# Performance work log

Hardware: AMD Instinct MI355X
Metric: run time of the kernel (lower is better)

Reference implementation:

```python
import jax, jax.numpy as jnp
import numpy as np
import math

B, S, D, H = 2, 2048, 1024, 16

def setup_inputs() -> dict:
    key = jax.random.key(0)
    ks = jax.random.split(key, 13)
    def lin(kw, kb, out_d, in_d):
        W = jax.random.normal(kw, (out_d, in_d), dtype=jnp.float32) * 0.02
        b = jax.random.normal(kb, (out_d,), dtype=jnp.float32) * 0.02
        return W, b
    Wq, bq = lin(ks[0], ks[1], D, D)
    Wk, bk = lin(ks[2], ks[3], D, D)
    Wv, bv = lin(ks[4], ks[5], D, D)
    Wo, bo = lin(ks[6], ks[7], D, D)
    query = jax.random.normal(ks[8], (B, S, D), dtype=jnp.float32)
    key_t = jax.random.normal(ks[9], (B, S, D), dtype=jnp.float32)
    value = jax.random.normal(ks[10], (B, S, D), dtype=jnp.float32)
    src_mask = jax.random.randint(ks[11], (B, S), 0, 2).astype(bool)  # True = masked out
    return {"query": query, "key": key_t, "value": value, "src_mask": src_mask,
            "Wq": Wq, "bq": bq, "Wk": Wk, "bk": bk, "Wv": Wv, "bv": bv,
            "Wo": Wo, "bo": bo, "nhead": H}

def reference(query, key, value, src_mask, Wq, bq, Wk, bk, Wv, bv, Wo, bo, nhead):
    b, s, d = query.shape
    hd = d // nhead
    scale = 1.0 / math.sqrt(hd)
    def split_heads(x):  # [b,s,d] -> [b,h,s,hd]
        return x.reshape(b, -1, nhead, hd).transpose(0, 2, 1, 3)
    q = split_heads(query @ Wq.T + bq)
    k = split_heads(key @ Wk.T + bk)
    v = split_heads(value @ Wv.T + bv)
    scores = jnp.einsum('bhqe,bhke->bhqk', q, k) * scale  # [b,h,s,s]
    # mask True -> -9e9, broadcast over heads and query positions (matches repeat)
    scores = jnp.where(src_mask[:, None, None, :], jnp.float32(-9e9), scores)
    probs = jax.nn.softmax(scores, axis=-1)
    # dropout is identity in eval mode
    out = jnp.einsum('bhqk,bhke->bhqe', probs, v)  # [b,h,s,hd]
    out = out.transpose(0, 2, 1, 3).reshape(b, s, d)
    out = out @ Wo.T + bo
    return out
```

## Files before the change

### kernel.cpp

```cpp
#include <hip/hip_runtime.h>
#include <hip/hip_bf16.h>
#include <cstdint>
#include <cstddef>

#define B_ 2
#define S_ 2048
#define D_ 1024
#define H_ 16
#define HD_ 64
#define M_ 4096

typedef __attribute__((ext_vector_type(8))) short short8;
typedef __attribute__((ext_vector_type(4))) short shortx4;
typedef __attribute__((ext_vector_type(4))) float floatx4;

__device__ __forceinline__ floatx4 mfma32(short8 a, short8 b, floatx4 c) {
    return __builtin_amdgcn_mfma_f32_16x16x32_bf16(a, b, c, 0, 0, 0);
}
__device__ __forceinline__ floatx4 mfma16(shortx4 a, shortx4 b, floatx4 c) {
    return __builtin_amdgcn_mfma_f32_16x16x16bf16_1k(a, b, c, 0, 0, 0);
}

__device__ __forceinline__ void gload_lds16(const __hip_bfloat16* g, __hip_bfloat16* lds_base) {
    __builtin_amdgcn_global_load_lds(
        (const __attribute__((address_space(1))) void*)g,
        (__attribute__((address_space(3))) void*)lds_base, 16, 0, 0);
}

__global__ __launch_bounds__(256) void cvt3_kernel(
    const float* __restrict__ a, const float* __restrict__ b, const float* __restrict__ c,
    __hip_bfloat16* __restrict__ dst, int n)
{
    const float* src = blockIdx.z == 0 ? a : blockIdx.z == 1 ? b : c;
    __hip_bfloat16* d = dst + (size_t)blockIdx.z * n;
    int i = (blockIdx.x * 256 + threadIdx.x) * 4;
    float4 v = *(const float4*)(src + i);
    union { __hip_bfloat16 h[4]; uint2 u; } cv;
    cv.h[0] = __float2bfloat16(v.x); cv.h[1] = __float2bfloat16(v.y);
    cv.h[2] = __float2bfloat16(v.z); cv.h[3] = __float2bfloat16(v.w);
    *(uint2*)(d + i) = cv.u;
}

__global__ __launch_bounds__(256) void cvt4_kernel(
    const float* __restrict__ a, const float* __restrict__ b,
    const float* __restrict__ c, const float* __restrict__ e,
    __hip_bfloat16* __restrict__ dst, int n)
{
    const float* src = blockIdx.z == 0 ? a : blockIdx.z == 1 ? b : blockIdx.z == 2 ? c : e;
    __hip_bfloat16* d = dst + (size_t)blockIdx.z * n;
    int i = (blockIdx.x * 256 + threadIdx.x) * 4;
    float4 v = *(const float4*)(src + i);
    union { __hip_bfloat16 h[4]; uint2 u; } cv;
    cv.h[0] = __float2bfloat16(v.x); cv.h[1] = __float2bfloat16(v.y);
    cv.h[2] = __float2bfloat16(v.z); cv.h[3] = __float2bfloat16(v.w);
    *(uint2*)(d + i) = cv.u;
}

template <int MODE>
__device__ __forceinline__ void gemm_core(
    const __hip_bfloat16* __restrict__ A,
    const __hip_bfloat16* __restrict__ W,
    const float* __restrict__ bias,
    void* __restrict__ Cout,
    __hip_bfloat16* __restrict__ smem,
    int m0, int n0, int N)
{
    __hip_bfloat16* As = smem;
    __hip_bfloat16* Bs = smem + 128 * 32;
    const int K = D_;
    const int tid  = threadIdx.x;
    const int wave = tid >> 6;
    const int lane = tid & 63;
    const int quad = lane >> 4;
    const int l15  = lane & 15;
    const int wm   = (wave & 1) * 64;
    const int wn   = (wave >> 1) * 64;
    const int srow = lane >> 2;
    const int scol = (lane & 3) * 8;

    floatx4 acc[4][4];
#pragma unroll
    for (int i = 0; i < 4; i++)
#pragma unroll
        for (int j = 0; j < 4; j++) {
            floatx4 z = {0.f, 0.f, 0.f, 0.f};
            acc[i][j] = z;
        }

    for (int k0 = 0; k0 < K; k0 += 32) {
        __syncthreads();
#pragma unroll
        for (int t = 0; t < 2; t++) {
            int r0 = wave * 32 + t * 16;
            gload_lds16(A + (size_t)(m0 + r0 + srow) * K + k0 + scol, As + r0 * 32);
            gload_lds16(W + (size_t)(n0 + r0 + srow) * K + k0 + scol, Bs + r0 * 32);
        }
        __syncthreads();

        short8 afr[4], bfr[4];
#pragma unroll
        for (int i = 0; i < 4; i++)
            afr[i] = *(const short8*)(As + (wm + i * 16 + l15) * 32 + quad * 8);
#pragma unroll
        for (int j = 0; j < 4; j++)
            bfr[j] = *(const short8*)(Bs + (wn + j * 16 + l15) * 32 + quad * 8);
#pragma unroll
        for (int i = 0; i < 4; i++)
#pragma unroll
            for (int j = 0; j < 4; j++)
                acc[i][j] = mfma32(afr[i], bfr[j], acc[i][j]);
    }

    if constexpr (MODE == 1) {
#pragma unroll
        for (int j = 0; j < 4; j++) {
            int col = n0 + wn + j * 16 + l15;
            int h = col >> 6, e = col & 63;
            float bv = bias[col];
#pragma unroll
            for (int i = 0; i < 4; i++) {
                int s0 = m0 + wm + i * 16 + quad * 4;
                int bb = s0 >> 11, sl = s0 & 2047;
                union { __hip_bfloat16 hx[4]; uint2 u; } pk;
#pragma unroll
                for (int r = 0; r < 4; r++)
                    pk.hx[r] = __float2bfloat16(acc[i][j][r] + bv);
                *(uint2*)((__hip_bfloat16*)Cout + (((size_t)bb * H_ + h) * HD_ + e) * S_ + sl) = pk.u;
            }
        }
    } else {
#pragma unroll
        for (int j = 0; j < 4; j++) {
            int col = n0 + wn + j * 16 + l15;
            float bv = bias[col];
#pragma unroll
            for (int i = 0; i < 4; i++) {
#pragma unroll
                for (int r = 0; r < 4; r++) {
                    int rowg = m0 + wm + i * 16 + quad * 4 + r;
                    ((__hip_bfloat16*)Cout)[(size_t)rowg * N + col] =
                        __float2bfloat16(acc[i][j][r] + bv);
                }
            }
        }
    }
}

__global__ __launch_bounds__(256) void qkv_gemm_kernel(
    const __hip_bfloat16* __restrict__ qb, const __hip_bfloat16* __restrict__ kb,
    const __hip_bfloat16* __restrict__ vb,
    const __hip_bfloat16* __restrict__ Wqb, const __hip_bfloat16* __restrict__ Wkb,
    const __hip_bfloat16* __restrict__ Wvb,
    const float* __restrict__ bq, const float* __restrict__ bk, const float* __restrict__ bv,
    __hip_bfloat16* __restrict__ Qp, __hip_bfloat16* __restrict__ Kp,
    __hip_bfloat16* __restrict__ Vt)
{
    __shared__ __hip_bfloat16 smem[2 * 128 * 32] __attribute__((aligned(16)));
    const int z = blockIdx.z;
    const __hip_bfloat16* A = z == 0 ? qb : z == 1 ? kb : vb;
    const __hip_bfloat16* W = z == 0 ? Wqb : z == 1 ? Wkb : Wvb;
    const float* bias = z == 0 ? bq : z == 1 ? bk : bv;
    int m0 = blockIdx.y * 128, n0 = blockIdx.x * 128;
    if (z < 2) gemm_core<0>(A, W, bias, z == 0 ? (void*)Qp : (void*)Kp, smem, m0, n0, D_);
    else       gemm_core<1>(A, W, bias, (void*)Vt, smem, m0, n0, D_);
}

__global__ __launch_bounds__(256) void oproj_gemm_kernel(
    const __hip_bfloat16* __restrict__ A, const __hip_bfloat16* __restrict__ W,
    const float* __restrict__ bias, float* __restrict__ out)
{
    __shared__ __hip_bfloat16 As[64 * 32]  __attribute__((aligned(16)));
    __shared__ __hip_bfloat16 Bs[128 * 32] __attribute__((aligned(16)));
    const int K = D_, N = D_;
    const int tid  = threadIdx.x;
    const int m0   = blockIdx.y * 64;
    const int n0   = blockIdx.x * 128;
    const int wave = tid >> 6;
    const int lane = tid & 63;
    const int quad = lane >> 4;
    const int l15  = lane & 15;
    const int wm   = (wave & 1) * 32;
    const int wn   = (wave >> 1) * 64;
    const int srow = lane >> 2;
    const int scol = (lane & 3) * 8;

    floatx4 acc[2][4];
#pragma unroll
    for (int i = 0; i < 2; i++)
#pragma unroll
        for (int j = 0; j < 4; j++) {
            floatx4 z = {0.f, 0.f, 0.f, 0.f};
            acc[i][j] = z;
        }

    for (int k0 = 0; k0 < K; k0 += 32) {
        __syncthreads();
        {
            int ra = wave * 16;
            gload_lds16(A + (size_t)(m0 + ra + srow) * K + k0 + scol, As + ra * 32);
#pragma unroll
            for (int t = 0; t < 2; t++) {
                int rb = wave * 32 + t * 16;
                gload_lds16(W + (size_t)(n0 + rb + srow) * K + k0 + scol, Bs + rb * 32);
            }
        }
        __syncthreads();

        short8 afr[2], bfr[4];
#pragma unroll
        for (int i = 0; i < 2; i++)
            afr[i] = *(const short8*)(As + (wm + i * 16 + l15) * 32 + quad * 8);
#pragma unroll
        for (int j = 0; j < 4; j++)
            bfr[j] = *(const short8*)(Bs + (wn + j * 16 + l15) * 32 + quad * 8);
#pragma unroll
        for (int i = 0; i < 2; i++)
#pragma unroll
            for (int j = 0; j < 4; j++)
                acc[i][j] = mfma32(afr[i], bfr[j], acc[i][j]);
    }

#pragma unroll
    for (int j = 0; j < 4; j++) {
        int col = n0 + wn + j * 16 + l15;
        float bv = bias[col];
#pragma unroll
        for (int i = 0; i < 2; i++) {
#pragma unroll
            for (int r = 0; r < 4; r++) {
                int rowg = m0 + wm + i * 16 + quad * 4 + r;
                out[(size_t)rowg * N + col] = acc[i][j][r] + bv;
            }
        }
    }
}

#define LDP 72
__global__ __launch_bounds__(512) void flash_attn_kernel(
    const __hip_bfloat16* __restrict__ Q,
    const __hip_bfloat16* __restrict__ Kp,
    const __hip_bfloat16* __restrict__ Vt,
    const int* __restrict__ mask,
    __hip_bfloat16* __restrict__ O)
{
    __shared__ __hip_bfloat16 Qs [128 * LDP] __attribute__((aligned(16)));
    __shared__ __hip_bfloat16 Ks [64 * LDP]  __attribute__((aligned(16)));
    __shared__ __hip_bfloat16 Vts[64 * LDP]  __attribute__((aligned(16)));

    const int tid  = threadIdx.x;
    const int q0   = blockIdx.x * 128;
    const int bh   = blockIdx.y;
    const int b    = bh >> 4;
    const int h    = bh & 15;
    const int wave = tid >> 6;
    const int lane = tid & 63;
    const int quad = lane >> 4;
    const int l15  = lane & 15;
    const float kSc = 0.18033688f;

    const size_t baseQ = ((size_t)b * S_ + q0) * D_ + (size_t)h * HD_;
#pragma unroll
    for (int c = tid; c < 1024; c += 512) {
        int row = c >> 3, kc = c & 7;
        *(uint4*)(Qs + row * LDP + kc * 8) = *(const uint4*)(Q + baseQ + (size_t)row * D_ + kc * 8);
    }
    __syncthreads();

    short8 qb[2];
    qb[0] = *(const short8*)(Qs + (wave * 16 + l15) * LDP + quad * 8);
    qb[1] = *(const short8*)(Qs + (wave * 16 + l15) * LDP + 32 + quad * 8);

    float lsum = 0.f;
    floatx4 o_acc[4];
#pragma unroll
    for (int ot = 0; ot < 4; ot++) {
        floatx4 z = {0.f, 0.f, 0.f, 0.f};
        o_acc[ot] = z;
    }

    const int* mrow = mask + b * S_;
    const __hip_bfloat16* VtBase = Vt + (size_t)bh * HD_ * S_;

    for (int kv0 = 0; kv0 < S_; kv0 += 64) {
        __syncthreads();
        const size_t baseK = ((size_t)b * S_ + kv0) * D_ + (size_t)h * HD_;
        {
            int row = tid >> 3, kc = tid & 7;
            *(uint4*)(Ks + row * LDP + kc * 8) =
                *(const uint4*)(Kp + baseK + (size_t)row * D_ + kc * 8);
            *(uint4*)(Vts + row * LDP + kc * 8) =
                *(const uint4*)(VtBase + (size_t)row * S_ + kv0 + kc * 8);
        }
        __syncthreads();

        int4 mq[4];
#pragma unroll
        for (int nt = 0; nt < 4; nt++)
            mq[nt] = *(const int4*)(mrow + kv0 + nt * 16 + quad * 4);

        floatx4 s_acc[4];
#pragma unroll
        for (int nt = 0; nt < 4; nt++) {
            short8 kb0 = *(const short8*)(Ks + (nt * 16 + l15) * LDP + quad * 8);
            short8 kb1 = *(const short8*)(Ks + (nt * 16 + l15) * LDP + 32 + quad * 8);
            floatx4 z = {0.f, 0.f, 0.f, 0.f};
            z = mfma32(kb0, qb[0], z);
            z = mfma32(kb1, qb[1], z);
            s_acc[nt] = z;
        }

        shortx4 pf[4];
#pragma unroll
        for (int nt = 0; nt < 4; nt++) {
            float pe0 = mq[nt].x ? 0.f : __builtin_amdgcn_exp2f(s_acc[nt][0] * kSc);
            float pe1 = mq[nt].y ? 0.f : __builtin_amdgcn_exp2f(s_acc[nt][1] * kSc);
            float pe2 = mq[nt].z ? 0.f : __builtin_amdgcn_exp2f(s_acc[nt][2] * kSc);
            float pe3 = mq[nt].w ? 0.f : __builtin_amdgcn_exp2f(s_acc[nt][3] * kSc);
            lsum += (pe0 + pe1) + (pe2 + pe3);
            union { shortx4 s4; __hip_bfloat162 b2[2]; } pk;
            pk.b2[0] = __float22bfloat162_rn({pe0, pe1});
            pk.b2[1] = __float22bfloat162_rn({pe2, pe3});
            pf[nt] = pk.s4;
        }

#pragma unroll
        for (int nt = 0; nt < 4; nt++) {
#pragma unroll
            for (int ot = 0; ot < 4; ot++) {
                shortx4 vb = *(const shortx4*)(Vts + (ot * 16 + l15) * LDP + nt * 16 + quad * 4);
                o_acc[ot] = mfma16(pf[nt], vb, o_acc[ot]);
            }
        }
    }

    lsum += __shfl_xor(lsum, 16);
    lsum += __shfl_xor(lsum, 32);

    const size_t baseO = ((size_t)b * S_ + q0) * D_ + (size_t)h * HD_;
#pragma unroll
    for (int r = 0; r < 4; r++) {
        float inv = 1.0f / __shfl(lsum, quad * 4 + r);
        int rowl = wave * 16 + quad * 4 + r;
#pragma unroll
        for (int ot = 0; ot < 4; ot++)
            O[baseO + (size_t)rowl * D_ + ot * 16 + l15] =
                __float2bfloat16(o_acc[ot][r] * inv);
    }
}

extern "C" void kernel_launch(void* const* d_in, const int* in_sizes, int n_in,
                              void* d_out, int out_size, void* d_ws, size_t ws_size,
                              hipStream_t stream) {
    const float* query = (const float*)d_in[0];
    const float* key   = (const float*)d_in[1];
    const float* value = (const float*)d_in[2];
    const int*   mask  = (const int*)d_in[3];
    const float* Wq    = (const float*)d_in[4];
    const float* bq    = (const float*)d_in[5];
    const float* Wk    = (const float*)d_in[6];
    const float* bk    = (const float*)d_in[7];
    const float* Wv    = (const float*)d_in[8];
    const float* bv    = (const float*)d_in[9];
    const float* Wo    = (const float*)d_in[10];
    const float* bo    = (const float*)d_in[11];
    float* out = (float*)d_out;

    const size_t SZ_IN = (size_t)M_ * D_;
    const size_t SZ_W  = (size_t)D_ * D_;
    __hip_bfloat16* qb  = (__hip_bfloat16*)d_ws;
    __hip_bfloat16* kb  = qb  + SZ_IN;
    __hip_bfloat16* vb  = kb  + SZ_IN;
    __hip_bfloat16* Wqb = vb  + SZ_IN;
    __hip_bfloat16* Wkb = Wqb + SZ_W;
    __hip_bfloat16* Wvb = Wkb + SZ_W;
    __hip_bfloat16* Wob = Wvb + SZ_W;
    __hip_bfloat16* Qp  = Wob + SZ_W;
    __hip_bfloat16* Kp  = Qp  + SZ_IN;
    __hip_bfloat16* Vt  = Kp  + SZ_IN;

    cvt3_kernel<<<dim3(SZ_IN / 1024, 1, 3), 256, 0, stream>>>(query, key, value, qb, (int)SZ_IN);
    cvt4_kernel<<<dim3(SZ_W / 1024, 1, 4), 256, 0, stream>>>(Wq, Wk, Wv, Wo, Wqb, (int)SZ_W);

    qkv_gemm_kernel<<<dim3(D_ / 128, M_ / 128, 3), 256, 0, stream>>>(
        qb, kb, vb, Wqb, Wkb, Wvb, bq, bk, bv, Qp, Kp, Vt);

    flash_attn_kernel<<<dim3(S_ / 128, B_ * H_), 512, 0, stream>>>(Qp, Kp, Vt, mask, Qp);

    oproj_gemm_kernel<<<dim3(D_ / 128, M_ / 64), 256, 0, stream>>>(Qp, Wob, bo, out);
}
```

Baseline: 242.4 us.

## Double-buffer K/V tiles in flash attention with register prefetch and 2 row-groups per wave

Rewrites the attention loop to prefetch the next K/V tile and mask into registers while computing the current one, storing into a second LDS buffer so each iteration needs one barrier instead of two. Block size drops from 512 to 256 threads, so each wave now handles two 16-row query groups and reuses each K/V LDS fragment across both. It also raises wave priority around the MFMA sections. The cost is more registers per thread and double the K/V LDS footprint, which may reduce occupancy.

```diff
diff --git a/kernel.cpp b/kernel.cpp
--- a/kernel.cpp
+++ b/kernel.cpp
@@ -236,16 +236,17 @@
 }
 
 #define LDP 72
-__global__ __launch_bounds__(512) void flash_attn_kernel(
+#define NT_ (S_ / 64)
+__global__ __launch_bounds__(256) void flash_attn_kernel(
     const __hip_bfloat16* __restrict__ Q,
     const __hip_bfloat16* __restrict__ Kp,
     const __hip_bfloat16* __restrict__ Vt,
     const int* __restrict__ mask,
     __hip_bfloat16* __restrict__ O)
 {
-    __shared__ __hip_bfloat16 Qs [128 * LDP] __attribute__((aligned(16)));
-    __shared__ __hip_bfloat16 Ks [64 * LDP]  __attribute__((aligned(16)));
-    __shared__ __hip_bfloat16 Vts[64 * LDP]  __attribute__((aligned(16)));
+    __shared__ __hip_bfloat16 Qs  [128 * LDP]    __attribute__((aligned(16)));
+    __shared__ __hip_bfloat16 KsB [2][64 * LDP]  __attribute__((aligned(16)));
+    __shared__ __hip_bfloat16 VtsB[2][64 * LDP]  __attribute__((aligned(16)));
 
     const int tid  = threadIdx.x;
     const int q0   = blockIdx.x * 128;
@@ -260,91 +261,132 @@
 
     const size_t baseQ = ((size_t)b * S_ + q0) * D_ + (size_t)h * HD_;
 #pragma unroll
-    for (int c = tid; c < 1024; c += 512) {
+    for (int c = tid; c < 1024; c += 256) {
         int row = c >> 3, kc = c & 7;
         *(uint4*)(Qs + row * LDP + kc * 8) = *(const uint4*)(Q + baseQ + (size_t)row * D_ + kc * 8);
     }
-    __syncthreads();
-
-    short8 qb[2];
-    qb[0] = *(const short8*)(Qs + (wave * 16 + l15) * LDP + quad * 8);
-    qb[1] = *(const short8*)(Qs + (wave * 16 + l15) * LDP + 32 + quad * 8);
-
-    float lsum = 0.f;
-    floatx4 o_acc[4];
-#pragma unroll
-    for (int ot = 0; ot < 4; ot++) {
-        floatx4 z = {0.f, 0.f, 0.f, 0.f};
-        o_acc[ot] = z;
-    }
 
     const int* mrow = mask + b * S_;
     const __hip_bfloat16* VtBase = Vt + (size_t)bh * HD_ * S_;
-
-    for (int kv0 = 0; kv0 < S_; kv0 += 64) {
-        __syncthreads();
-        const size_t baseK = ((size_t)b * S_ + kv0) * D_ + (size_t)h * HD_;
-        {
-            int row = tid >> 3, kc = tid & 7;
-            *(uint4*)(Ks + row * LDP + kc * 8) =
-                *(const uint4*)(Kp + baseK + (size_t)row * D_ + kc * 8);
-            *(uint4*)(Vts + row * LDP + kc * 8) =
-                *(const uint4*)(VtBase + (size_t)row * S_ + kv0 + kc * 8);
-        }
-        __syncthreads();
+    const size_t baseKrow = (size_t)b * S_ * D_ + (size_t)h * HD_;
+
+    const int r0  = tid >> 3;
+    const int r1  = r0 + 32;
+    const int kc0 = (tid & 7) * 8;
+
+    uint4 kreg0, kreg1, vreg0, vreg1;
+    int4  mreg[4];
+
+    auto issue = [&](int kv0) {
+        kreg0 = *(const uint4*)(Kp + baseKrow + (size_t)(kv0 + r0) * D_ + kc0);
+        kreg1 = *(const uint4*)(Kp + baseKrow + (size_t)(kv0 + r1) * D_ + kc0);
+        vreg0 = *(const uint4*)(VtBase + (size_t)r0 * S_ + kv0 + kc0);
+        vreg1 = *(const uint4*)(VtBase + (size_t)r1 * S_ + kv0 + kc0);
+#pragma unroll
+        for (int nt = 0; nt < 4; nt++)
+            mreg[nt] = *(const int4*)(mrow + kv0 + nt * 16 + quad * 4);
+    };
+    auto commit = [&](int pb) {
+        *(uint4*)(KsB[pb]  + r0 * LDP + kc0) = kreg0;
+        *(uint4*)(KsB[pb]  + r1 * LDP + kc0) = kreg1;
+        *(uint4*)(VtsB[pb] + r0 * LDP + kc0) = vreg0;
+        *(uint4*)(VtsB[pb] + r1 * LDP + kc0) = vreg1;
+    };
+
+    issue(0);
+    commit(0);
+    __syncthreads();
+
+    short8 qb[2][2];
+#pragma unroll
+    for (int g = 0; g < 2; g++) {
+        qb[g][0] = *(const short8*)(Qs + (wave * 32 + g * 16 + l15) * LDP + quad * 8);
+        qb[g][1] = *(const short8*)(Qs + (wave * 32 + g * 16 + l15) * LDP + 32 + quad * 8);
+    }
+
+    float lsum[2] = {0.f, 0.f};
+    floatx4 o_acc[2][4];
+#pragma unroll
+    for (int g = 0; g < 2; g++)
+#pragma unroll
+        for (int ot = 0; ot < 4; ot++) {
+            floatx4 z = {0.f, 0.f, 0.f, 0.f};
+            o_acc[g][ot] = z;
+        }
+
+    for (int t = 0; t < NT_; ++t) {
+        if (t) __syncthreads();
 
         int4 mq[4];
 #pragma unroll
-        for (int nt = 0; nt < 4; nt++)
-            mq[nt] = *(const int4*)(mrow + kv0 + nt * 16 + quad * 4);
-
-        floatx4 s_acc[4];
+        for (int nt = 0; nt < 4; nt++) mq[nt] = mreg[nt];
+
+        if (t + 1 < NT_) issue((t + 1) * 64);
+
+        const __hip_bfloat16* Ks  = KsB [t & 1];
+        const __hip_bfloat16* Vts = VtsB[t & 1];
+
+        floatx4 s_acc[2][4];
+        __builtin_amdgcn_s_setprio(1);
 #pragma unroll
         for (int nt = 0; nt < 4; nt++) {
             short8 kb0 = *(const short8*)(Ks + (nt * 16 + l15) * LDP + quad * 8);
             short8 kb1 = *(const short8*)(Ks + (nt * 16 + l15) * LDP + 32 + quad * 8);
-            floatx4 z = {0.f, 0.f, 0.f, 0.f};
-            z = mfma32(kb0, qb[0], z);
-            z = mfma32(kb1, qb[1], z);
-            s_acc[nt] = z;
-        }
-
-        shortx4 pf[4];
-#pragma unroll
-        for (int nt = 0; nt < 4; nt++) {
-            float pe0 = mq[nt].x ? 0.f : __builtin_amdgcn_exp2f(s_acc[nt][0] * kSc);
-            float pe1 = mq[nt].y ? 0.f : __builtin_amdgcn_exp2f(s_acc[nt][1] * kSc);
-            float pe2 = mq[nt].z ? 0.f : __builtin_amdgcn_exp2f(s_acc[nt][2] * kSc);
-            float pe3 = mq[nt].w ? 0.f : __builtin_amdgcn_exp2f(s_acc[nt][3] * kSc);
-            lsum += (pe0 + pe1) + (pe2 + pe3);
-            union { shortx4 s4; __hip_bfloat162 b2[2]; } pk;
-            pk.b2[0] = __float22bfloat162_rn({pe0, pe1});
-            pk.b2[1] = __float22bfloat162_rn({pe2, pe3});
-            pf[nt] = pk.s4;
-        }
-
-#pragma unroll
-        for (int nt = 0; nt < 4; nt++) {
+#pragma unroll
+            for (int g = 0; g < 2; g++) {
+                floatx4 z = {0.f, 0.f, 0.f, 0.f};
+                z = mfma32(kb0, qb[g][0], z);
+                z = mfma32(kb1, qb[g][1], z);
+                s_acc[g][nt] = z;
+            }
+        }
+        __builtin_amdgcn_s_setprio(0);
+
+        shortx4 pf[2][4];
+#pragma unroll
+        for (int g = 0; g < 2; g++)
+#pragma unroll
+            for (int nt = 0; nt < 4; nt++) {
+                float pe0 = mq[nt].x ? 0.f : __builtin_amdgcn_exp2f(s_acc[g][nt][0] * kSc);
+                float pe1 = mq[nt].y ? 0.f : __builtin_amdgcn_exp2f(s_acc[g][nt][1] * kSc);
+                float pe2 = mq[nt].z ? 0.f : __builtin_amdgcn_exp2f(s_acc[g][nt][2] * kSc);
+                float pe3 = mq[nt].w ? 0.f : __builtin_amdgcn_exp2f(s_acc[g][nt][3] * kSc);
+                lsum[g] += (pe0 + pe1) + (pe2 + pe3);
+                union { shortx4 s4; __hip_bfloat162 b2[2]; } pk;
+                pk.b2[0] = __float22bfloat162_rn({pe0, pe1});
+                pk.b2[1] = __float22bfloat162_rn({pe2, pe3});
+                pf[g][nt] = pk.s4;
+            }
+
+        __builtin_amdgcn_s_setprio(1);
+#pragma unroll
+        for (int nt = 0; nt < 4; nt++)
 #pragma unroll
             for (int ot = 0; ot < 4; ot++) {
                 shortx4 vb = *(const shortx4*)(Vts + (ot * 16 + l15) * LDP + nt * 16 + quad * 4);
-                o_acc[ot] = mfma16(pf[nt], vb, o_acc[ot]);
-            }
-        }
-    }
-
-    lsum += __shfl_xor(lsum, 16);
-    lsum += __shfl_xor(lsum, 32);
-
-    const size_t baseO = ((size_t)b * S_ + q0) * D_ + (size_t)h * HD_;
-#pragma unroll
-    for (int r = 0; r < 4; r++) {
-        float inv = 1.0f / __shfl(lsum, quad * 4 + r);
-        int rowl = wave * 16 + quad * 4 + r;
-#pragma unroll
-        for (int ot = 0; ot < 4; ot++)
-            O[baseO + (size_t)rowl * D_ + ot * 16 + l15] =
-                __float2bfloat16(o_acc[ot][r] * inv);
+                o_acc[0][ot] = mfma16(pf[0][nt], vb, o_acc[0][ot]);
+                o_acc[1][ot] = mfma16(pf[1][nt], vb, o_acc[1][ot]);
+            }
+        __builtin_amdgcn_s_setprio(0);
+
+        if (t + 1 < NT_) commit((t + 1) & 1);
+    }
+
+    const size_t baseO = baseQ;
+#pragma unroll
+    for (int g = 0; g < 2; g++) {
+        float ls = lsum[g];
+        ls += __shfl_xor(ls, 16);
+        ls += __shfl_xor(ls, 32);
+#pragma unroll
+        for (int r = 0; r < 4; r++) {
+            float inv = 1.0f / __shfl(ls, quad * 4 + r);
+            int rowl = wave * 32 + g * 16 + quad * 4 + r;
+#pragma unroll
+            for (int ot = 0; ot < 4; ot++)
+                O[baseO + (size_t)rowl * D_ + ot * 16 + l15] =
+                    __float2bfloat16(o_acc[g][ot][r] * inv);
+        }
     }
 }
 
@@ -384,7 +426,7 @@
     qkv_gemm_kernel<<<dim3(D_ / 128, M_ / 128, 3), 256, 0, stream>>>(
         qb, kb, vb, Wqb, Wkb, Wvb, bq, bk, bv, Qp, Kp, Vt);
 
-    flash_attn_kernel<<<dim3(S_ / 128, B_ * H_), 512, 0, stream>>>(Qp, Kp, Vt, mask, Qp);
+    flash_attn_kernel<<<dim3(S_ / 128, B_ * H_), 256, 0, stream>>>(Qp, Kp, Vt, mask, Qp);
 
     oproj_gemm_kernel<<<dim3(D_ / 128, M_ / 64), 256, 0, stream>>>(Qp, Wob, bo, out);
 }
```

Measured after the change: 239.1 us. Within noise of the previous version (-1.4%).

## Double-buffer K/V tiles in flash attention with register prefetch

Applied to the files above, without the earlier changes.

The attention loop now uses two LDS buffers for K and V^T tiles. Global loads for the next tile, including the mask, go into registers before the current tile's MFMAs and are written to the other buffer afterwards, which drops one barrier per iteration. MFMA sections are also wrapped in s_setprio to raise wave priority. The aim is to hide global-load latency behind compute, at the cost of extra LDS and registers.

```diff
diff --git a/kernel.cpp b/kernel.cpp
--- a/kernel.cpp
+++ b/kernel.cpp
@@ -236,6 +236,7 @@
 }
 
 #define LDP 72
+#define NT_ (S_ / 64)
 __global__ __launch_bounds__(512) void flash_attn_kernel(
     const __hip_bfloat16* __restrict__ Q,
     const __hip_bfloat16* __restrict__ Kp,
@@ -243,9 +244,9 @@
     const int* __restrict__ mask,
     __hip_bfloat16* __restrict__ O)
 {
-    __shared__ __hip_bfloat16 Qs [128 * LDP] __attribute__((aligned(16)));
-    __shared__ __hip_bfloat16 Ks [64 * LDP]  __attribute__((aligned(16)));
-    __shared__ __hip_bfloat16 Vts[64 * LDP]  __attribute__((aligned(16)));
+    __shared__ __hip_bfloat16 Qs  [128 * LDP]    __attribute__((aligned(16)));
+    __shared__ __hip_bfloat16 KsB [2][64 * LDP]  __attribute__((aligned(16)));
+    __shared__ __hip_bfloat16 VtsB[2][64 * LDP]  __attribute__((aligned(16)));
 
     const int tid  = threadIdx.x;
     const int q0   = blockIdx.x * 128;
@@ -264,6 +265,31 @@
         int row = c >> 3, kc = c & 7;
         *(uint4*)(Qs + row * LDP + kc * 8) = *(const uint4*)(Q + baseQ + (size_t)row * D_ + kc * 8);
     }
+
+    const int* mrow = mask + b * S_;
+    const __hip_bfloat16* VtBase = Vt + (size_t)bh * HD_ * S_;
+    const size_t baseKrow = (size_t)b * S_ * D_ + (size_t)h * HD_;
+
+    const int r0  = tid >> 3;
+    const int kc0 = (tid & 7) * 8;
+
+    uint4 kreg, vreg;
+    int4  mreg[4];
+
+    auto issue = [&](int kv0) {
+        kreg = *(const uint4*)(Kp + baseKrow + (size_t)(kv0 + r0) * D_ + kc0);
+        vreg = *(const uint4*)(VtBase + (size_t)r0 * S_ + kv0 + kc0);
+#pragma unroll
+        for (int nt = 0; nt < 4; nt++)
+            mreg[nt] = *(const int4*)(mrow + kv0 + nt * 16 + quad * 4);
+    };
+    auto commit = [&](int pb) {
+        *(uint4*)(KsB[pb]  + r0 * LDP + kc0) = kreg;
+        *(uint4*)(VtsB[pb] + r0 * LDP + kc0) = vreg;
+    };
+
+    issue(0);
+    commit(0);
     __syncthreads();
 
     short8 qb[2];
@@ -278,27 +304,20 @@
         o_acc[ot] = z;
     }
 
-    const int* mrow = mask + b * S_;
-    const __hip_bfloat16* VtBase = Vt + (size_t)bh * HD_ * S_;
-
-    for (int kv0 = 0; kv0 < S_; kv0 += 64) {
-        __syncthreads();
-        const size_t baseK = ((size_t)b * S_ + kv0) * D_ + (size_t)h * HD_;
-        {
-            int row = tid >> 3, kc = tid & 7;
-            *(uint4*)(Ks + row * LDP + kc * 8) =
-                *(const uint4*)(Kp + baseK + (size_t)row * D_ + kc * 8);
-            *(uint4*)(Vts + row * LDP + kc * 8) =
-                *(const uint4*)(VtBase + (size_t)row * S_ + kv0 + kc * 8);
-        }
-        __syncthreads();
+    for (int t = 0; t < NT_; ++t) {
+        if (t) __syncthreads();
 
         int4 mq[4];
 #pragma unroll
-        for (int nt = 0; nt < 4; nt++)
-            mq[nt] = *(const int4*)(mrow + kv0 + nt * 16 + quad * 4);
+        for (int nt = 0; nt < 4; nt++) mq[nt] = mreg[nt];
+
+        if (t + 1 < NT_) issue((t + 1) * 64);
+
+        const __hip_bfloat16* Ks  = KsB [t & 1];
+        const __hip_bfloat16* Vts = VtsB[t & 1];
 
         floatx4 s_acc[4];
+        __builtin_amdgcn_s_setprio(1);
 #pragma unroll
         for (int nt = 0; nt < 4; nt++) {
             short8 kb0 = *(const short8*)(Ks + (nt * 16 + l15) * LDP + quad * 8);
@@ -308,6 +327,7 @@
             z = mfma32(kb1, qb[1], z);
             s_acc[nt] = z;
         }
+        __builtin_amdgcn_s_setprio(0);
 
         shortx4 pf[4];
 #pragma unroll
@@ -323,6 +343,7 @@
             pf[nt] = pk.s4;
         }
 
+        __builtin_amdgcn_s_setprio(1);
 #pragma unroll
         for (int nt = 0; nt < 4; nt++) {
 #pragma unroll
@@ -331,12 +352,15 @@
                 o_acc[ot] = mfma16(pf[nt], vb, o_acc[ot]);
             }
         }
+        __builtin_amdgcn_s_setprio(0);
+
+        if (t + 1 < NT_) commit((t + 1) & 1);
     }
 
     lsum += __shfl_xor(lsum, 16);
     lsum += __shfl_xor(lsum, 32);
 
-    const size_t baseO = ((size_t)b * S_ + q0) * D_ + (size_t)h * HD_;
+    const size_t baseO = baseQ;
 #pragma unroll
     for (int r = 0; r < 4; r++) {
         float inv = 1.0f / __shfl(lsum, quad * 4 + r);
```

New measurement: 241.9 us. About the same (-0.2%).
